# Performance work log

Measured on AMD Instinct MI355X. Metric: run time of the kernel, lower is better.

Reference implementation:

```python
import jax, jax.numpy as jnp
import numpy as np

B, NPG, H, HEADS, L, E, IN_DIM, FREQ = 4, 256, 128, 4, 6, 65536, 5, 256
N = B * NPG
C = H // HEADS  # per-head channels = 32


def _w(key, shape, fan_in):
    return jax.random.normal(key, shape, jnp.float32) * (fan_in ** -0.5)


def _ln(x):  # LayerNorm, elementwise_affine=False, eps=1e-5
    mu = jnp.mean(x, axis=-1, keepdims=True)
    var = jnp.mean((x - mu) ** 2, axis=-1, keepdims=True)
    return (x - mu) / jnp.sqrt(var + 1e-5)


def setup_inputs() -> dict:
    key = jax.random.key(0)
    ks = jax.random.split(key, 40)
    x = jax.random.normal(ks[0], (N, IN_DIM), jnp.float32)
    # edges constrained within each graph
    kg = jnp.repeat(jnp.arange(B), E // B)
    src = jax.random.randint(ks[1], (E,), 0, NPG) + kg * NPG
    dst = jax.random.randint(ks[2], (E,), 0, NPG) + kg * NPG
    edge_index = jnp.stack([src, dst]).astype(jnp.int32)
    batch = jnp.repeat(jnp.arange(B), NPG).astype(jnp.int32)
    time_matrix = jax.random.normal(ks[3], (N, N), jnp.float32)
    p = {}
    p['Wn'] = _w(ks[4], (IN_DIM, H), IN_DIM); p['bn'] = jnp.zeros((H,), jnp.float32)
    p['Wee'] = _w(ks[5], (1, 1), 1); p['bee'] = jnp.zeros((1,), jnp.float32)
    p['Wt1'] = _w(ks[6], (FREQ, H), FREQ); p['bt1'] = jnp.zeros((H,), jnp.float32)
    p['Wt2'] = _w(ks[7], (H, H), H); p['bt2'] = jnp.zeros((H,), jnp.float32)
    p['Wa'] = _w(ks[8], (L, H, 4 * H), H); p['ba'] = jnp.zeros((L, 4 * H), jnp.float32)
    p['Wq'] = _w(ks[9], (L, H, H), H); p['bq'] = jnp.zeros((L, H), jnp.float32)
    p['Wk'] = _w(ks[10], (L, H, H), H); p['bk'] = jnp.zeros((L, H), jnp.float32)
    p['Wv'] = _w(ks[11], (L, H, H), H); p['bv'] = jnp.zeros((L, H), jnp.float32)
    p['We'] = _w(ks[12], (L, 1, H), 1)  # lin_edge, bias=False in PyG
    p['Wskip'] = _w(ks[13], (L, H, H), H); p['bskip'] = jnp.zeros((L, H), jnp.float32)
    p['Wf1'] = _w(ks[14], (L, H, 2 * H), H); p['bf1'] = jnp.zeros((L, 2 * H), jnp.float32)
    p['Wf2'] = _w(ks[15], (L, 2 * H, H), 2 * H); p['bf2'] = jnp.zeros((L, H), jnp.float32)
    p['Wb'] = _w(ks[16], (H, H, H), H); p['bb'] = jnp.zeros((H,), jnp.float32)
    p['Wm1'] = _w(ks[17], (H, H), H); p['bm1'] = jnp.zeros((H,), jnp.float32)
    p['Wm2'] = _w(ks[18], (H, 4), H); p['bm2'] = jnp.zeros((4,), jnp.float32)
    return {'x': x, 'edge_index': edge_index, 'batch': batch, 't': 50,
            'time_matrix': time_matrix, **p}


def reference(x, edge_index, batch, t, time_matrix,
              Wn, bn, Wee, bee, Wt1, bt1, Wt2, bt2,
              Wa, ba, Wq, bq, Wk, bk, Wv, bv, We, Wskip, bskip,
              Wf1, bf1, Wf2, bf2, Wb, bb, Wm1, bm1, Wm2, bm2):
    h = x @ Wn + bn  # [N,H]
    # sinusoidal timestep embedding (dim=FREQ)
    half = FREQ // 2
    freqs = jnp.exp(-jnp.log(jnp.float32(10000.0)) * jnp.arange(half, dtype=jnp.float32) / half)
    targs = jnp.float32(t) * freqs
    emb = jnp.concatenate([jnp.cos(targs), jnp.sin(targs)])[None, :]  # [1,FREQ]
    t_emb = jax.nn.silu(emb @ Wt1 + bt1) @ Wt2 + bt2  # [1,H]
    t_mod = jax.nn.silu(t_emb)

    src, dst = edge_index[0], edge_index[1]
    edge_attr = time_matrix[src, dst][:, None] @ Wee + bee  # [E,1]

    inv_sqrt_c = jnp.float32(1.0 / np.sqrt(C))
    for l in range(L):
        ss = t_mod @ Wa[l] + ba[l]  # [1,4H]
        sh_msa, sc_msa, sh_mlp, sc_mlp = jnp.split(ss, 4, axis=1)
        hn = _ln(h) * (1 + sc_msa) + sh_msa
        # TransformerConv: gather per-edge Q/K/V, softmax over incoming edges of dst
        q = (hn @ Wq[l] + bq[l]).reshape(N, HEADS, C)
        k = (hn @ Wk[l] + bk[l]).reshape(N, HEADS, C)
        v = (hn @ Wv[l] + bv[l]).reshape(N, HEADS, C)
        e = (edge_attr @ We[l]).reshape(E, HEADS, C)
        kj = k[src] + e
        alpha = jnp.sum(q[dst] * kj, axis=-1) * inv_sqrt_c  # [E,HEADS]
        m = jax.ops.segment_max(alpha, dst, num_segments=N)
        a = jnp.exp(alpha - m[dst])
        s = jax.ops.segment_sum(a, dst, num_segments=N)
        a = a / (s[dst] + 1e-16)
        msg = (v[src] + e) * a[..., None]  # [E,HEADS,C]
        attn_out = jax.ops.segment_sum(msg, dst, num_segments=N).reshape(N, H)
        attn_out = attn_out + hn @ Wskip[l] + bskip[l]  # root/skip connection
        h = h + attn_out
        hn = _ln(h) * (1 + sc_mlp) + sh_mlp
        h = h + (jax.nn.gelu(hn @ Wf1[l] + bf1[l], approximate=False) @ Wf2[l] + bf2[l])

    # to_dense_batch: all graphs have NPG nodes -> reshape, full mask
    hd = h.reshape(B, NPG, H)
    # nn.Bilinear: pair[b,i,j,o] = h[b,i] @ Wb[o] @ h[b,j] + bb[o]
    tmp = jnp.einsum('bik,okl->biol', hd, Wb)  # [B,n,H,H]
    pair = jnp.einsum('biol,bjl->bijo', tmp, hd) + bb  # [B,n,n,H]
    logits = jax.nn.silu(pair @ Wm1 + bm1) @ Wm2 + bm2  # [B,n,n,4]
    return logits
```

## Files before the change

kernel.cpp:

```cpp
#include <hip/hip_runtime.h>
#include <math.h>

#define N_NODES 1024
#define HDIM 128
#define EDGES 65536
#define LAYERS 6

typedef __attribute__((ext_vector_type(8))) short bf16x8;
typedef __attribute__((ext_vector_type(4))) float f32x4;

#define OFF_H     0
#define OFF_Q     131072
#define OFF_K     262144
#define OFF_V     393216
#define OFF_SKP   524288
#define OFF_G     655360
#define OFF_SS    917504
#define OFF_EA    920576
#define OFF_CVEC  986112
#define OFF_INT   986240
#define OFF_M     1054912
#define OFF_U     3152064
#define OFF_MT    11540672
#define OFF_HB    12589248
#define OFF_WB    12654912

#define WM1T_OFF  786432

__device__ __forceinline__ float silu_f(float x) { return x / (1.f + expf(-x)); }
__device__ __forceinline__ float frcp(float x) { return __builtin_amdgcn_rcpf(x); }

__device__ __forceinline__ unsigned short f2bf(float f) {
    unsigned int u = __float_as_uint(f);
    u += 0x7FFFu + ((u >> 16) & 1u);
    return (unsigned short)(u >> 16);
}
__device__ __forceinline__ float bf2f(unsigned short s) {
    return __uint_as_float(((unsigned int)s) << 16);
}

__global__ __launch_bounds__(256) void k_ssf(const void* tptr,
    const float* __restrict__ Wt1, const float* __restrict__ bt1,
    const float* __restrict__ Wt2, const float* __restrict__ bt2,
    const float* __restrict__ bb, const float* __restrict__ Wm1, const float* __restrict__ bm1,
    const float* __restrict__ Wa, const float* __restrict__ ba,
    float* __restrict__ ss_all, float* __restrict__ cvec)
{
    __shared__ float emb_s[256];
    __shared__ float part[2][128];
    __shared__ float tmp1_s[128];
    __shared__ float tmod_s[128];
    int tid = threadIdx.x;
    int iv = *(const int*)tptr;
    float fv = __int_as_float(iv);
    float tval = (iv > -1000000 && iv < 1000000) ? (float)iv : fv;
    {
        int fi = tid & 127;
        float fr = expf(-logf(10000.f) * (float)fi / 128.f);
        float ta = tval * fr;
        emb_s[tid] = (tid < 128) ? cosf(ta) : sinf(ta);
    }
    __syncthreads();
    {
        int col = tid & 127, sl = tid >> 7;
        float p = 0.f;
#pragma unroll 8
        for (int i = sl * 128; i < sl * 128 + 128; i++) p += emb_s[i] * Wt1[i * 128 + col];
        part[sl][col] = p;
    }
    __syncthreads();
    if (tid < 128) tmp1_s[tid] = silu_f(bt1[tid] + part[0][tid] + part[1][tid]);
    __syncthreads();
    {
        int col = tid & 127, sl = tid >> 7;
        float p = 0.f;
#pragma unroll 8
        for (int i = sl * 64; i < sl * 64 + 64; i++) p += tmp1_s[i] * Wt2[i * 128 + col];
        part[sl][col] = p;
    }
    __syncthreads();
    if (tid < 128) tmod_s[tid] = silu_f(bt2[tid] + part[0][tid] + part[1][tid]);
    __syncthreads();
    {
        int idx = blockIdx.x * 256 + tid;
        int l = idx >> 9, j = idx & 511;
        float a = ba[l * 512 + j];
        const float* w = Wa + l * 65536 + j;
#pragma unroll 4
        for (int k = 0; k < 128; k++) a += tmod_s[k] * w[k * 512];
        ss_all[idx] = a;
    }
    if (blockIdx.x == 0) {
        {
            int col = tid & 127, sl = tid >> 7;
            float p = 0.f;
#pragma unroll 8
            for (int i = sl * 64; i < sl * 64 + 64; i++) p += bb[i] * Wm1[i * 128 + col];
            part[sl][col] = p;
        }
        __syncthreads();
        if (tid < 128) cvec[tid] = bm1[tid] + part[0][tid] + part[1][tid];
    }
}

__global__ __launch_bounds__(256) void k_wtrans(
    const float* __restrict__ Wq, const float* __restrict__ Wk,
    const float* __restrict__ Wv, const float* __restrict__ Wsk,
    const float* __restrict__ Wf1, const float* __restrict__ Wf2,
    const float* __restrict__ Wm1, short* __restrict__ WT)
{
    __shared__ __align__(16) short T[64][80];
    int t = blockIdx.x;
    int tid = threadIdx.x;
    const float* src; short* dst; int K, N, kt, nt;
    if (t < 96) {
        int mat = t >> 2, sub = t & 3;
        int l = mat >> 2, m = mat & 3;
        src = (m == 0 ? Wq : m == 1 ? Wk : m == 2 ? Wv : Wsk) + l * 16384;
        dst = WT + (size_t)mat * 16384;
        K = 128; N = 128; kt = sub >> 1; nt = sub & 1;
    } else if (t < 144) {
        int i = t - 96; int l = i >> 3, sub = i & 7;
        src = Wf1 + l * 32768;
        dst = WT + 24 * 16384 + (size_t)l * 32768;
        K = 128; N = 256; kt = sub & 1; nt = sub >> 1;
    } else if (t < 192) {
        int i = t - 144; int l = i >> 3, sub = i & 7;
        src = Wf2 + l * 32768;
        dst = WT + 24 * 16384 + 6 * 32768 + (size_t)l * 32768;
        K = 256; N = 128; kt = sub >> 1; nt = sub & 1;
    } else {
        int sub = t - 192;
        src = Wm1;
        dst = WT + WM1T_OFF;
        K = 128; N = 128; kt = sub >> 1; nt = sub & 1;
    }
    int k0 = kt * 64, n0 = nt * 64;
    for (int p = 0; p < 16; p++) {
        int idx = p * 256 + tid;
        int kk = idx >> 6, nn = idx & 63;
        T[nn][kk] = (short)f2bf(src[(k0 + kk) * N + n0 + nn]);
    }
    __syncthreads();
    for (int p = 0; p < 2; p++) {
        int idx = p * 256 + tid;
        int nn = idx >> 3, sq = idx & 7;
        *(int4*)&dst[(size_t)(n0 + nn) * K + k0 + sq * 8] = *(const int4*)&T[nn][sq * 8];
    }
}

__global__ __launch_bounds__(256) void k_inpedge(const float* __restrict__ x,
    const float* __restrict__ Wn, const float* __restrict__ bn, float* __restrict__ h,
    const int* __restrict__ ei, const float* __restrict__ tm,
    const float* __restrict__ Wee, const float* __restrict__ bee,
    float* __restrict__ ea, int* __restrict__ deg)
{
    int bid = blockIdx.x;
    int tid = threadIdx.x;
    if (bid < 512) {
        int idx = bid * 256 + tid;
        int i = idx >> 7, j = idx & 127;
        float acc = bn[j];
#pragma unroll
        for (int kk = 0; kk < 5; kk++) acc += x[i * 5 + kk] * Wn[kk * 128 + j];
        h[idx] = acc;
    } else {
        int e = (bid - 512) * 256 + tid;
        int s = ei[e], d = ei[EDGES + e];
        ea[e] = tm[s * N_NODES + d] * Wee[0] + bee[0];
        atomicAdd(&deg[d], 1);
    }
}

__global__ __launch_bounds__(1024) void k_scan(const int* __restrict__ deg, int* __restrict__ rowptr)
{
    __shared__ int tmp[1024];
    int tid = threadIdx.x;
    tmp[tid] = deg[tid];
    __syncthreads();
    for (int off = 1; off < 1024; off <<= 1) {
        int vv = (tid >= off) ? tmp[tid - off] : 0;
        __syncthreads();
        tmp[tid] += vv;
        __syncthreads();
    }
    rowptr[tid + 1] = tmp[tid];
    if (tid == 0) rowptr[0] = 0;
}

__global__ __launch_bounds__(256) void k_scatter(const int* __restrict__ ei,
    const int* __restrict__ rowptr, int* __restrict__ cursor, int* __restrict__ eorder)
{
    int e = blockIdx.x * 256 + threadIdx.x;
    int d = ei[EDGES + e];
    int pos = atomicAdd(&cursor[d], 1);
    eorder[rowptr[d] + pos] = e;
}

__global__ __launch_bounds__(128) void k_sort2(const int* __restrict__ rowptr,
    int* __restrict__ eorder, const int* __restrict__ ei, const float* __restrict__ ea,
    int* __restrict__ src_csr, float* __restrict__ ea_csr)
{
    __shared__ int key[256];
    int node = blockIdx.x;
    int tid = threadIdx.x;
    int beg = rowptr[node], end = rowptr[node + 1];
    int n = end - beg;
    if (n <= 256) {
        for (int i = tid; i < 256; i += 128) key[i] = (i < n) ? eorder[beg + i] : 0x7FFFFFFF;
        __syncthreads();
        for (int k = 2; k <= 256; k <<= 1) {
            for (int j = k >> 1; j > 0; j >>= 1) {
                int i = ((tid / j) * 2 * j) + (tid % j);
                int l = i + j;
                bool up = ((i & k) == 0);
                int a = key[i], b = key[l];
                if ((a > b) == up) { key[i] = b; key[l] = a; }
                __syncthreads();
            }
        }
        for (int i = tid; i < n; i += 128) {
            int e = key[i];
            src_csr[beg + i] = ei[e];
            ea_csr[beg + i] = ea[e];
        }
    } else {
        if (tid == 0) {
            for (int i = beg + 1; i < end; ++i) {
                int kk = eorder[i];
                int j = i - 1;
                while (j >= beg && eorder[j] > kk) { eorder[j + 1] = eorder[j]; --j; }
                eorder[j + 1] = kk;
            }
        }
        __syncthreads();
        for (int i = tid; i < n; i += 128) {
            int e = eorder[beg + i];
            src_csr[beg + i] = ei[e];
            ea_csr[beg + i] = ea[e];
        }
    }
}

__global__ __launch_bounds__(256) void k_qkvs(const float* __restrict__ h,
    const float* __restrict__ ss, const short* __restrict__ WT, int layer,
    const float* __restrict__ bq, const float* __restrict__ bk,
    const float* __restrict__ bv, const float* __restrict__ bsk,
    float* __restrict__ q, short* __restrict__ kb16, short* __restrict__ vb16,
    float* __restrict__ skp)
{
    __shared__ __align__(16) short As[16][136];
    __shared__ float shs[128], scs[128];
    int tid = threadIdx.x;
    int r0 = blockIdx.x * 16;
    if (tid < 128) { shs[tid] = ss[tid]; scs[tid] = ss[128 + tid]; }
    __syncthreads();
    {
        int row = tid >> 4, o = tid & 15;
        const float* hr = h + (size_t)(r0 + row) * 128 + o * 8;
        float s = 0.f, s2 = 0.f;
#pragma unroll
        for (int j = 0; j < 2; j++) {
            float4 vv = *(const float4*)&hr[j * 4];
            s += vv.x + vv.y + vv.z + vv.w;
            s2 += vv.x * vv.x + vv.y * vv.y + vv.z * vv.z + vv.w * vv.w;
        }
        s += __shfl_xor(s, 1, 64); s2 += __shfl_xor(s2, 1, 64);
        s += __shfl_xor(s, 2, 64); s2 += __shfl_xor(s2, 2, 64);
        s += __shfl_xor(s, 4, 64); s2 += __shfl_xor(s2, 4, 64);
        s += __shfl_xor(s, 8, 64); s2 += __shfl_xor(s2, 8, 64);
        float mu = s * (1.f / 128.f);
        float var = s2 * (1.f / 128.f) - mu * mu;
        float rs = rsqrtf(var + 1e-5f);
#pragma unroll
        for (int j = 0; j < 2; j++) {
            float4 vv = *(const float4*)&hr[j * 4];
            int cb = o * 8 + j * 4;
            short4 o4;
            o4.x = (short)f2bf((vv.x - mu) * rs * (1.f + scs[cb])     + shs[cb]);
            o4.y = (short)f2bf((vv.y - mu) * rs * (1.f + scs[cb + 1]) + shs[cb + 1]);
            o4.z = (short)f2bf((vv.z - mu) * rs * (1.f + scs[cb + 2]) + shs[cb + 2]);
            o4.w = (short)f2bf((vv.w - mu) * rs * (1.f + scs[cb + 3]) + shs[cb + 3]);
            *(short4*)&As[row][cb] = o4;
        }
    }
    __syncthreads();
    int w = tid >> 6, lane = tid & 63, c = lane & 15, g = lane >> 4;
    const short* Wm = WT + (size_t)(layer * 4 + w) * 16384;
    f32x4 acc[8] = {};
#pragma unroll
    for (int kq = 0; kq < 4; kq++) {
        int ko = kq * 32 + g * 8;
        bf16x8 a0 = *(const bf16x8*)&As[c][ko];
#pragma unroll
        for (int nt = 0; nt < 8; nt++) {
            bf16x8 bfr = *(const bf16x8*)&Wm[(size_t)(nt * 16 + c) * 128 + ko];
            acc[nt] = __builtin_amdgcn_mfma_f32_16x16x32_bf16(a0, bfr, acc[nt], 0, 0, 0);
        }
    }
    if (w == 0) {
#pragma unroll
        for (int nt = 0; nt < 8; nt++) {
            int n = nt * 16 + c;
            float bv2 = bq[n];
#pragma unroll
            for (int r = 0; r < 4; r++)
                q[(size_t)(r0 + g * 4 + r) * 128 + n] = acc[nt][r] + bv2;
        }
    } else if (w == 1) {
#pragma unroll
        for (int nt = 0; nt < 8; nt++) {
            int n = nt * 16 + c;
            float bv2 = bk[n];
#pragma unroll
            for (int r = 0; r < 4; r++)
                kb16[(size_t)(r0 + g * 4 + r) * 128 + n] = (short)f2bf(acc[nt][r] + bv2);
        }
    } else if (w == 2) {
#pragma unroll
        for (int nt = 0; nt < 8; nt++) {
            int n = nt * 16 + c;
            float bv2 = bv[n];
#pragma unroll
            for (int r = 0; r < 4; r++)
                vb16[(size_t)(r0 + g * 4 + r) * 128 + n] = (short)f2bf(acc[nt][r] + bv2);
        }
    } else {
#pragma unroll
        for (int nt = 0; nt < 8; nt++) {
            int n = nt * 16 + c;
            float bv2 = bsk[n];
#pragma unroll
            for (int r = 0; r < 4; r++)
                skp[(size_t)(r0 + g * 4 + r) * 128 + n] = acc[nt][r] + bv2;
        }
    }
}

__global__ __launch_bounds__(256) void k_ffn(float* __restrict__ h,
    const short* __restrict__ WT, int layer,
    const float* __restrict__ bf1, const float* __restrict__ bf2,
    const float* __restrict__ ss2, short* __restrict__ hb, int last)
{
    __shared__ __align__(16) short As[16][136];
    __shared__ __align__(16) short Gs[16][264];
    __shared__ float shs[128], scs[128];
    int tid = threadIdx.x;
    int r0 = blockIdx.x * 16;
    if (tid < 128) { shs[tid] = ss2[tid]; scs[tid] = ss2[128 + tid]; }
    __syncthreads();
    {
        int row = tid >> 4, o = tid & 15;
        const float* hr = h + (size_t)(r0 + row) * 128 + o * 8;
        float s = 0.f, s2 = 0.f;
#pragma unroll
        for (int j = 0; j < 2; j++) {
            float4 vv = *(const float4*)&hr[j * 4];
            s += vv.x + vv.y + vv.z + vv.w;
            s2 += vv.x * vv.x + vv.y * vv.y + vv.z * vv.z + vv.w * vv.w;
        }
        s += __shfl_xor(s, 1, 64); s2 += __shfl_xor(s2, 1, 64);
        s += __shfl_xor(s, 2, 64); s2 += __shfl_xor(s2, 2, 64);
        s += __shfl_xor(s, 4, 64); s2 += __shfl_xor(s2, 4, 64);
        s += __shfl_xor(s, 8, 64); s2 += __shfl_xor(s2, 8, 64);
        float mu = s * (1.f / 128.f);
        float var = s2 * (1.f / 128.f) - mu * mu;
        float rs = rsqrtf(var + 1e-5f);
#pragma unroll
        for (int j = 0; j < 2; j++) {
            float4 vv = *(const float4*)&hr[j * 4];
            int cb = o * 8 + j * 4;
            short4 o4;
            o4.x = (short)f2bf((vv.x - mu) * rs * (1.f + scs[cb])     + shs[cb]);
            o4.y = (short)f2bf((vv.y - mu) * rs * (1.f + scs[cb + 1]) + shs[cb + 1]);
            o4.z = (short)f2bf((vv.z - mu) * rs * (1.f + scs[cb + 2]) + shs[cb + 2]);
            o4.w = (short)f2bf((vv.w - mu) * rs * (1.f + scs[cb + 3]) + shs[cb + 3]);
            *(short4*)&As[row][cb] = o4;
        }
    }
    __syncthreads();
    int w = tid >> 6, lane = tid & 63, c = lane & 15, g = lane >> 4;
    const short* W1 = WT + 24 * 16384 + (size_t)layer * 32768;
    const short* W2 = WT + 24 * 16384 + 6 * 32768 + (size_t)layer * 32768;
    {
        f32x4 acc[4] = {};
#pragma unroll
        for (int kq = 0; kq < 4; kq++) {
            int ko = kq * 32 + g * 8;
            bf16x8 a0 = *(const bf16x8*)&As[c][ko];
#pragma unroll
            for (int nt = 0; nt < 4; nt++) {
                bf16x8 bfr = *(const bf16x8*)&W1[(size_t)(w * 64 + nt * 16 + c) * 128 + ko];
                acc[nt] = __builtin_amdgcn_mfma_f32_16x16x32_bf16(a0, bfr, acc[nt], 0, 0, 0);
            }
        }
#pragma unroll
        for (int nt = 0; nt < 4; nt++) {
            int n = w * 64 + nt * 16 + c;
            float bv = bf1[n];
#pragma unroll
            for (int r = 0; r < 4; r++) {
                float y = acc[nt][r] + bv;
                float gl = 0.5f * y * (1.f + erff(y * 0.70710678118654752f));
                Gs[g * 4 + r][n] = (short)f2bf(gl);
            }
        }
    }
    __syncthreads();
    {
        f32x4 acc2[2] = {};
#pragma unroll
        for (int kq = 0; kq < 8; kq++) {
            int ko = kq * 32 + g * 8;
            bf16x8 a0 = *(const bf16x8*)&Gs[c][ko];
#pragma unroll
            for (int nt2 = 0; nt2 < 2; nt2++) {
                bf16x8 bfr = *(const bf16x8*)&W2[(size_t)(w * 32 + nt2 * 16 + c) * 256 + ko];
                acc2[nt2] = __builtin_amdgcn_mfma_f32_16x16x32_bf16(a0, bfr, acc2[nt2], 0, 0, 0);
            }
        }
#pragma unroll
        for (int nt2 = 0; nt2 < 2; nt2++) {
            int n = w * 32 + nt2 * 16 + c;
            float bv = bf2[n];
#pragma unroll
            for (int r = 0; r < 4; r++) {
                int i = r0 + g * 4 + r;
                float nv = h[(size_t)i * 128 + n] + acc2[nt2][r] + bv;
                h[(size_t)i * 128 + n] = nv;
                if (last) hb[(size_t)i * 128 + n] = (short)f2bf(nv);
            }
        }
    }
}

__global__ __launch_bounds__(256) void k_attn(const float* __restrict__ q,
    const short* __restrict__ kb16, const short* __restrict__ vb16,
    const float* __restrict__ skp, float* __restrict__ h,
    const int* __restrict__ src_csr, const float* __restrict__ ea_csr,
    const float* __restrict__ We_l, const int* __restrict__ rowptr)
{
    __shared__ float ms[3][64], ssb[3][64], a0s[3][64], a1s[3][64];
    int tid = threadIdx.x;
    int wid = tid >> 6;
    int lane = tid & 63;
    int node = blockIdx.x;
    int c0 = lane * 2;
    float2 q2 = *(const float2*)&q[node * 128 + c0];
    float we0 = We_l[c0], we1 = We_l[c0 + 1];
    int beg = rowptr[node], end = rowptr[node + 1];
    int n = end - beg;
    int tb = beg + (n * wid) / 4;
    int te = beg + (n * (wid + 1)) / 4;
    float m = -INFINITY, s = 0.f, a0 = 0.f, a1 = 0.f;
    const float isc = 0.17677669529663687f;

    int t = tb;
    for (; t + 3 < te; t += 4) {
        int sn0 = src_csr[t],     sn1 = src_csr[t + 1];
        int sn2 = src_csr[t + 2], sn3 = src_csr[t + 3];
        float e0 = ea_csr[t],     e1 = ea_csr[t + 1];
        float e2 = ea_csr[t + 2], e3 = ea_csr[t + 3];
        ushort2 ku0 = *(const ushort2*)&kb16[sn0 * 128 + c0];
        ushort2 ku1 = *(const ushort2*)&kb16[sn1 * 128 + c0];
        ushort2 ku2 = *(const ushort2*)&kb16[sn2 * 128 + c0];
        ushort2 ku3 = *(const ushort2*)&kb16[sn3 * 128 + c0];
        ushort2 vu0 = *(const ushort2*)&vb16[sn0 * 128 + c0];
        ushort2 vu1 = *(const ushort2*)&vb16[sn1 * 128 + c0];
        ushort2 vu2 = *(const ushort2*)&vb16[sn2 * 128 + c0];
        ushort2 vu3 = *(const ushort2*)&vb16[sn3 * 128 + c0];
        float p0 = q2.x * (bf2f(ku0.x) + e0 * we0) + q2.y * (bf2f(ku0.y) + e0 * we1);
        float p1 = q2.x * (bf2f(ku1.x) + e1 * we0) + q2.y * (bf2f(ku1.y) + e1 * we1);
        float p2 = q2.x * (bf2f(ku2.x) + e2 * we0) + q2.y * (bf2f(ku2.y) + e2 * we1);
        float p3 = q2.x * (bf2f(ku3.x) + e3 * we0) + q2.y * (bf2f(ku3.y) + e3 * we1);
        p0 += __shfl_xor(p0, 1, 16); p1 += __shfl_xor(p1, 1, 16);
        p2 += __shfl_xor(p2, 1, 16); p3 += __shfl_xor(p3, 1, 16);
        p0 += __shfl_xor(p0, 2, 16); p1 += __shfl_xor(p1, 2, 16);
        p2 += __shfl_xor(p2, 2, 16); p3 += __shfl_xor(p3, 2, 16);
        p0 += __shfl_xor(p0, 4, 16); p1 += __shfl_xor(p1, 4, 16);
        p2 += __shfl_xor(p2, 4, 16); p3 += __shfl_xor(p3, 4, 16);
        p0 += __shfl_xor(p0, 8, 16); p1 += __shfl_xor(p1, 8, 16);
        p2 += __shfl_xor(p2, 8, 16); p3 += __shfl_xor(p3, 8, 16);
        {
            float al = p0 * isc;
            float mn = fmaxf(m, al);
            float scale = __expf(m - mn), wq = __expf(al - mn);
            s = s * scale + wq;
            a0 = a0 * scale + wq * (bf2f(vu0.x) + e0 * we0);
            a1 = a1 * scale + wq * (bf2f(vu0.y) + e0 * we1);
            m = mn;
        }
        {
            float al = p1 * isc;
            float mn = fmaxf(m, al);
            float scale = __expf(m - mn), wq = __expf(al - mn);
            s = s * scale + wq;
            a0 = a0 * scale + wq * (bf2f(vu1.x) + e1 * we0);
            a1 = a1 * scale + wq * (bf2f(vu1.y) + e1 * we1);
            m = mn;
        }
        {
            float al = p2 * isc;
            float mn = fmaxf(m, al);
            float scale = __expf(m - mn), wq = __expf(al - mn);
            s = s * scale + wq;
            a0 = a0 * scale + wq * (bf2f(vu2.x) + e2 * we0);
            a1 = a1 * scale + wq * (bf2f(vu2.y) + e2 * we1);
            m = mn;
        }
        {
            float al = p3 * isc;
            float mn = fmaxf(m, al);
            float scale = __expf(m - mn), wq = __expf(al - mn);
            s = s * scale + wq;
            a0 = a0 * scale + wq * (bf2f(vu3.x) + e3 * we0);
            a1 = a1 * scale + wq * (bf2f(vu3.y) + e3 * we1);
            m = mn;
        }
    }
    for (; t < te; ++t) {
        int sn = src_csr[t];
        float eav = ea_csr[t];
        ushort2 ku = *(const ushort2*)&kb16[sn * 128 + c0];
        ushort2 vu = *(const ushort2*)&vb16[sn * 128 + c0];
        float part = q2.x * (bf2f(ku.x) + eav * we0) + q2.y * (bf2f(ku.y) + eav * we1);
        part += __shfl_xor(part, 1, 16);
        part += __shfl_xor(part, 2, 16);
        part += __shfl_xor(part, 4, 16);
        part += __shfl_xor(part, 8, 16);
        float alpha = part * isc;
        float mn = fmaxf(m, alpha);
        float scale = __expf(m - mn), wq = __expf(alpha - mn);
        s = s * scale + wq;
        a0 = a0 * scale + wq * (bf2f(vu.x) + eav * we0);
        a1 = a1 * scale + wq * (bf2f(vu.y) + eav * we1);
        m = mn;
    }
    if (wid > 0) {
        ms[wid - 1][lane] = m; ssb[wid - 1][lane] = s;
        a0s[wid - 1][lane] = a0; a1s[wid - 1][lane] = a1;
    }
    __syncthreads();
    if (wid == 0) {
#pragma unroll
        for (int p = 0; p < 3; p++) {
            float mB = ms[p][lane], sB = ssb[p][lane];
            float b0 = a0s[p][lane], b1 = a1s[p][lane];
            float mm = fmaxf(m, mB);
            float eA = (m  > -1e30f) ? __expf(m  - mm) : 0.f;
            float eB = (mB > -1e30f) ? __expf(mB - mm) : 0.f;
            s = s * eA + sB * eB;
            a0 = a0 * eA + b0 * eB;
            a1 = a1 * eA + b1 * eB;
            m = mm;
        }
        float inv = (s > 0.f) ? 1.f / (s + 1e-16f) : 0.f;
        int o = node * 128 + c0;
        h[o]     += skp[o]     + a0 * inv;
        h[o + 1] += skp[o + 1] + a1 * inv;
    }
}

__global__ __launch_bounds__(256) void k_mprep(const float* __restrict__ Wb,
    const short* __restrict__ WT, float* __restrict__ M)
{
    __shared__ __align__(16) short Bls[128][136];
    int tid = threadIdx.x;
    int k = blockIdx.x;
    const short* Wm1T = WT + WM1T_OFF;
    {
        int lq = (tid & 31) * 4;
        int ob = tid >> 5;
        for (int it = 0; it < 16; it++) {
            int o = it * 8 + ob;
            float4 vv = *(const float4*)&Wb[(size_t)o * 16384 + k * 128 + lq];
            Bls[lq][o]     = (short)f2bf(vv.x);
            Bls[lq + 1][o] = (short)f2bf(vv.y);
            Bls[lq + 2][o] = (short)f2bf(vv.z);
            Bls[lq + 3][o] = (short)f2bf(vv.w);
        }
    }
    __syncthreads();
    int w = tid >> 6, lane = tid & 63, c = lane & 15, g = lane >> 4;
    f32x4 acc[2][8] = {};
#pragma unroll
    for (int kq = 0; kq < 4; kq++) {
        int ko = kq * 32 + g * 8;
        bf16x8 a0 = *(const bf16x8*)&Wm1T[(size_t)(w * 32 + c) * 128 + ko];
        bf16x8 a1 = *(const bf16x8*)&Wm1T[(size_t)(w * 32 + 16 + c) * 128 + ko];
#pragma unroll
        for (int nt = 0; nt < 8; nt++) {
            bf16x8 b = *(const bf16x8*)&Bls[nt * 16 + c][ko];
            acc[0][nt] = __builtin_amdgcn_mfma_f32_16x16x32_bf16(a0, b, acc[0][nt], 0, 0, 0);
            acc[1][nt] = __builtin_amdgcn_mfma_f32_16x16x32_bf16(a1, b, acc[1][nt], 0, 0, 0);
        }
    }
    float* Mk = M + (size_t)k * 16384;
#pragma unroll
    for (int it = 0; it < 2; it++)
#pragma unroll
        for (int nt = 0; nt < 8; nt++)
#pragma unroll
            for (int r = 0; r < 4; r++) {
                int m = w * 32 + it * 16 + g * 4 + r;
                int l = nt * 16 + c;
                Mk[m * 128 + l] = acc[it][nt][r];
            }
}

__global__ __launch_bounds__(256) void k_mtrans(const float* __restrict__ M,
                                                short* __restrict__ Mt)
{
    __shared__ __align__(16) short Ts[64][136];
    int tid = threadIdx.x;
    int n0 = blockIdx.x * 64;
    for (int p = 0; p < 32; p++) {
        int idx = p * 256 + tid;
        int k = idx >> 6, nn = idx & 63;
        Ts[nn][k] = (short)f2bf(M[(size_t)k * 16384 + n0 + nn]);
    }
    __syncthreads();
    for (int p = 0; p < 4; p++) {
        int idx = p * 256 + tid;
        int nn = idx >> 4, s = idx & 15;
        *(int4*)&Mt[(size_t)(n0 + nn) * 128 + s * 8] = *(const int4*)&Ts[nn][s * 8];
    }
}

__global__ __launch_bounds__(256) void k_p1(const short* __restrict__ hb,
    const short* __restrict__ Mt, short* __restrict__ U)
{
    __shared__ __align__(16) short As[128][72];
    __shared__ __align__(16) short Bs[128][72];
    int tid = threadIdx.x;
    int n0 = blockIdx.x * 128;
    int i0 = blockIdx.y * 128;
    int w = tid >> 6, lane = tid & 63, c = lane & 15, g = lane >> 4;
    f32x4 acc[2][8] = {};
    for (int kh = 0; kh < 2; kh++) {
        __syncthreads();
        for (int idx = tid; idx < 1024; idx += 256) {
            int r = idx >> 3, s = idx & 7;
            *(int4*)&As[r][s * 8] = *(const int4*)&hb[(i0 + r) * 128 + kh * 64 + s * 8];
            *(int4*)&Bs[r][s * 8] = *(const int4*)&Mt[(size_t)(n0 + r) * 128 + kh * 64 + s * 8];
        }
        __syncthreads();
#pragma unroll
        for (int kk = 0; kk < 2; kk++) {
            int ko = kk * 32 + g * 8;
            bf16x8 a0 = *(const bf16x8*)&As[w * 32 + c][ko];
            bf16x8 a1 = *(const bf16x8*)&As[w * 32 + 16 + c][ko];
#pragma unroll
            for (int nt = 0; nt < 8; nt++) {
                bf16x8 b = *(const bf16x8*)&Bs[nt * 16 + c][ko];
                acc[0][nt] = __builtin_amdgcn_mfma_f32_16x16x32_bf16(a0, b, acc[0][nt], 0, 0, 0);
                acc[1][nt] = __builtin_amdgcn_mfma_f32_16x16x32_bf16(a1, b, acc[1][nt], 0, 0, 0);
            }
        }
    }
#pragma unroll
    for (int it = 0; it < 2; it++)
#pragma unroll
        for (int nt = 0; nt < 8; nt++)
#pragma unroll
            for (int r = 0; r < 4; r++) {
                int i = i0 + w * 32 + it * 16 + g * 4 + r;
                int n = n0 + nt * 16 + c;
                U[(size_t)i * 16384 + n] = (short)f2bf(acc[it][nt][r]);
            }
}

__global__ __launch_bounds__(256) void k_p2(const short* __restrict__ hb,
    const short* __restrict__ U, const float* __restrict__ cvec,
    const float* __restrict__ Wm2, const float* __restrict__ bm2,
    float* __restrict__ out)
{
    __shared__ __align__(16) short Us[128][128];
    __shared__ float cvs[128];
    __shared__ float w2s[128][4];
    int tid = threadIdx.x;
    int i = blockIdx.x;
    int jb = blockIdx.y;
    int b = i >> 8;
    int w = tid >> 6, lane = tid & 63, c = lane & 15, g = lane >> 4;
    if (tid < 128) {
        cvs[tid] = cvec[tid];
        *(float4*)&w2s[tid][0] = *(const float4*)&Wm2[tid * 4];
    }
    bf16x8 hf[2][4];
    {
        const short* hrow = hb + (size_t)(b * 256 + jb * 128 + w * 32 + c) * 128;
#pragma unroll
        for (int jt = 0; jt < 2; jt++)
#pragma unroll
            for (int kq = 0; kq < 4; kq++)
                hf[jt][kq] = *(const bf16x8*)(hrow + jt * 16 * 128 + kq * 32 + g * 8);
    }
    for (int idx = tid; idx < 2048; idx += 256) {
        int r = idx >> 4, s = idx & 15;
        int col = (s * 8) ^ ((r & 7) << 3);
        *(int4*)&Us[r][col] = *(const int4*)&U[(size_t)i * 16384 + r * 128 + s * 8];
    }
    __syncthreads();
    f32x4 acc[2][8] = {};
#pragma unroll
    for (int kq = 0; kq < 4; kq++) {
        int ko = kq * 32 + g * 8;
#pragma unroll
        for (int mt = 0; mt < 8; mt++) {
            int row = mt * 16 + c;
            int col = ko ^ ((row & 7) << 3);
            bf16x8 uv = *(const bf16x8*)&Us[row][col];
            acc[0][mt] = __builtin_amdgcn_mfma_f32_16x16x32_bf16(uv, hf[0][kq], acc[0][mt], 0, 0, 0);
            acc[1][mt] = __builtin_amdgcn_mfma_f32_16x16x32_bf16(uv, hf[1][kq], acc[1][mt], 0, 0, 0);
        }
    }
    float4 bmv = *(const float4*)&bm2[0];
#pragma unroll
    for (int jt = 0; jt < 2; jt++) {
        float p0 = 0.f, p1 = 0.f, p2 = 0.f, p3 = 0.f;
#pragma unroll
        for (int mt = 0; mt < 8; mt++) {
#pragma unroll
            for (int r = 0; r < 4; r++) {
                int m = mt * 16 + g * 4 + r;
                float y = acc[jt][mt][r] + cvs[m];
                float sv = y * frcp(1.f + __expf(-y));
                p0 += sv * w2s[m][0]; p1 += sv * w2s[m][1];
                p2 += sv * w2s[m][2]; p3 += sv * w2s[m][3];
            }
        }
        p0 += __shfl_xor(p0, 16, 64); p1 += __shfl_xor(p1, 16, 64);
        p2 += __shfl_xor(p2, 16, 64); p3 += __shfl_xor(p3, 16, 64);
        p0 += __shfl_xor(p0, 32, 64); p1 += __shfl_xor(p1, 32, 64);
        p2 += __shfl_xor(p2, 32, 64); p3 += __shfl_xor(p3, 32, 64);
        if (g == 0) {
            int j = jb * 128 + w * 32 + jt * 16 + c;
            float4 o4 = { p0 + bmv.x, p1 + bmv.y, p2 + bmv.z, p3 + bmv.w };
            *(float4*)&out[((size_t)i * 256 + j) * 4] = o4;
        }
    }
}

extern "C" void kernel_launch(void* const* d_in, const int* in_sizes, int n_in,
                              void* d_out, int out_size, void* d_ws, size_t ws_size,
                              hipStream_t stream)
{
    const float* x   = (const float*)d_in[0];
    const int*   ei  = (const int*)d_in[1];
    const void*  tptr= d_in[3];
    const float* tm  = (const float*)d_in[4];
    const float* Wn  = (const float*)d_in[5];
    const float* bn  = (const float*)d_in[6];
    const float* Wee = (const float*)d_in[7];
    const float* bee = (const float*)d_in[8];
    const float* Wt1 = (const float*)d_in[9];
    const float* bt1 = (const float*)d_in[10];
    const float* Wt2 = (const float*)d_in[11];
    const float* bt2 = (const float*)d_in[12];
    const float* Wa  = (const float*)d_in[13];
    const float* ba  = (const float*)d_in[14];
    const float* Wq  = (const float*)d_in[15];
    const float* bq  = (const float*)d_in[16];
    const float* Wk  = (const float*)d_in[17];
    const float* bk  = (const float*)d_in[18];
    const float* Wv  = (const float*)d_in[19];
    const float* bv  = (const float*)d_in[20];
    const float* We  = (const float*)d_in[21];
    const float* Wsk = (const float*)d_in[22];
    const float* bsk = (const float*)d_in[23];
    const float* Wf1 = (const float*)d_in[24];
    const float* bf1 = (const float*)d_in[25];
    const float* Wf2 = (const float*)d_in[26];
    const float* bf2 = (const float*)d_in[27];
    const float* Wb  = (const float*)d_in[28];
    const float* bb  = (const float*)d_in[29];
    const float* Wm1 = (const float*)d_in[30];
    const float* bm1 = (const float*)d_in[31];
    const float* Wm2 = (const float*)d_in[32];
    const float* bm2 = (const float*)d_in[33];
    float* out = (float*)d_out;
    float* ws = (float*)d_ws;

    float* h    = ws + OFF_H;
    float* qb   = ws + OFF_Q;
    short* kb16 = (short*)(ws + OFF_K);
    short* vb16 = (short*)(ws + OFF_V);
    float* skp  = ws + OFF_SKP;
    float* ss   = ws + OFF_SS;
    float* ea   = ws + OFF_EA;
    float* cvec = ws + OFF_CVEC;
    int* iws    = (int*)(ws + OFF_INT);
    int* deg    = iws;
    int* cursor = iws + 1024;
    int* rowptr = iws + 2048;
    int* eorder = iws + 3073;
    int* src_csr   = (int*)(ws + OFF_G);
    float* ea_csr  = ws + OFF_G + 65536;
    float* Mst  = ws + OFF_M;
    short* Ub   = (short*)(ws + OFF_U);
    short* Mtb  = (short*)(ws + OFF_MT);
    short* hbb  = (short*)(ws + OFF_HB);
    short* WT   = (short*)(ws + OFF_WB);

    hipMemsetAsync(deg, 0, 2048 * sizeof(int), stream);
    k_ssf<<<12, 256, 0, stream>>>(tptr, Wt1, bt1, Wt2, bt2, bb, Wm1, bm1, Wa, ba, ss, cvec);
    k_wtrans<<<196, 256, 0, stream>>>(Wq, Wk, Wv, Wsk, Wf1, Wf2, Wm1, WT);
    k_inpedge<<<768, 256, 0, stream>>>(x, Wn, bn, h, ei, tm, Wee, bee, ea, deg);
    k_scan<<<1, 1024, 0, stream>>>(deg, rowptr);
    k_scatter<<<256, 256, 0, stream>>>(ei, rowptr, cursor, eorder);
    k_sort2<<<1024, 128, 0, stream>>>(rowptr, eorder, ei, ea, src_csr, ea_csr);

    for (int l = 0; l < LAYERS; l++) {
        const float* ssl = ss + l * 512;
        k_qkvs<<<64, 256, 0, stream>>>(h, ssl, WT, l,
            bq + l * 128, bk + l * 128, bv + l * 128, bsk + l * 128,
            qb, kb16, vb16, skp);
        k_attn<<<1024, 256, 0, stream>>>(qb, kb16, vb16, skp, h, src_csr, ea_csr,
                                         We + l * 128, rowptr);
        k_ffn<<<64, 256, 0, stream>>>(h, WT, l, bf1 + l * 256, bf2 + l * 128,
                                      ssl + 256, hbb, l == LAYERS - 1);
    }

    k_mprep<<<128, 256, 0, stream>>>(Wb, WT, Mst);
    k_mtrans<<<256, 256, 0, stream>>>(Mst, Mtb);
    k_p1<<<dim3(128, 8), 256, 0, stream>>>(hbb, Mtb, Ub);
    k_p2<<<dim3(1024, 2), 256, 0, stream>>>(hbb, Ub, cvec, Wm2, bm2, out);
}
```

Measured before the change: 276.3 us.

## Merge setup kernels and weight-product prep into one launch, swap grid axes

Folds the time-embedding/scale-shift kernel, the weight transpose kernel, the input/edge kernel, and the bilinear M-prep kernel into one multi-role kernel. Block index selects the role. The M-prep branch now builds its own transposed bf16 Wm1 tile in shared memory instead of reading the transposed weights, which removes its dependency on the transpose blocks. Grid axes of the two pair kernels are swapped so that consecutive blocks walk the inner dimension. This saves three launches, but the fused kernel reserves ~68KB of shared memory for every block, which can lower occupancy for the lightweight elementwise blocks.

```diff
diff --git a/kernel.cpp b/kernel.cpp
--- a/kernel.cpp
+++ b/kernel.cpp
@@ -39,136 +39,184 @@
     return __uint_as_float(((unsigned int)s) << 16);
 }
 
-__global__ __launch_bounds__(256) void k_ssf(const void* tptr,
+__global__ __launch_bounds__(256) void k_setup_all(const void* tptr,
     const float* __restrict__ Wt1, const float* __restrict__ bt1,
     const float* __restrict__ Wt2, const float* __restrict__ bt2,
     const float* __restrict__ bb, const float* __restrict__ Wm1, const float* __restrict__ bm1,
     const float* __restrict__ Wa, const float* __restrict__ ba,
-    float* __restrict__ ss_all, float* __restrict__ cvec)
-{
-    __shared__ float emb_s[256];
-    __shared__ float part[2][128];
-    __shared__ float tmp1_s[128];
-    __shared__ float tmod_s[128];
+    float* __restrict__ ss_all, float* __restrict__ cvec,
+    const float* __restrict__ Wq, const float* __restrict__ Wk,
+    const float* __restrict__ Wv, const float* __restrict__ Wsk,
+    const float* __restrict__ Wf1, const float* __restrict__ Wf2,
+    short* __restrict__ WT,
+    const float* __restrict__ x, const float* __restrict__ Wn, const float* __restrict__ bn,
+    float* __restrict__ h, const int* __restrict__ ei, const float* __restrict__ tm,
+    const float* __restrict__ Wee, const float* __restrict__ bee,
+    float* __restrict__ ea, int* __restrict__ deg,
+    const float* __restrict__ Wb, float* __restrict__ M)
+{
+    __shared__ __align__(16) char smem[69632];
+    int bid = blockIdx.x;
     int tid = threadIdx.x;
-    int iv = *(const int*)tptr;
-    float fv = __int_as_float(iv);
-    float tval = (iv > -1000000 && iv < 1000000) ? (float)iv : fv;
-    {
-        int fi = tid & 127;
-        float fr = expf(-logf(10000.f) * (float)fi / 128.f);
-        float ta = tval * fr;
-        emb_s[tid] = (tid < 128) ? cosf(ta) : sinf(ta);
-    }
-    __syncthreads();
-    {
-        int col = tid & 127, sl = tid >> 7;
-        float p = 0.f;
-#pragma unroll 8
-        for (int i = sl * 128; i < sl * 128 + 128; i++) p += emb_s[i] * Wt1[i * 128 + col];
-        part[sl][col] = p;
-    }
-    __syncthreads();
-    if (tid < 128) tmp1_s[tid] = silu_f(bt1[tid] + part[0][tid] + part[1][tid]);
-    __syncthreads();
-    {
-        int col = tid & 127, sl = tid >> 7;
-        float p = 0.f;
-#pragma unroll 8
-        for (int i = sl * 64; i < sl * 64 + 64; i++) p += tmp1_s[i] * Wt2[i * 128 + col];
-        part[sl][col] = p;
-    }
-    __syncthreads();
-    if (tid < 128) tmod_s[tid] = silu_f(bt2[tid] + part[0][tid] + part[1][tid]);
-    __syncthreads();
-    {
-        int idx = blockIdx.x * 256 + tid;
-        int l = idx >> 9, j = idx & 511;
-        float a = ba[l * 512 + j];
-        const float* w = Wa + l * 65536 + j;
-#pragma unroll 4
-        for (int k = 0; k < 128; k++) a += tmod_s[k] * w[k * 512];
-        ss_all[idx] = a;
-    }
-    if (blockIdx.x == 0) {
+
+    if (bid < 12) {
+        float* emb_s  = (float*)smem;
+        float* part   = emb_s + 256;
+        float* tmp1_s = part + 256;
+        float* tmod_s = tmp1_s + 128;
+        int iv = *(const int*)tptr;
+        float fv = __int_as_float(iv);
+        float tval = (iv > -1000000 && iv < 1000000) ? (float)iv : fv;
+        {
+            int fi = tid & 127;
+            float fr = expf(-logf(10000.f) * (float)fi / 128.f);
+            float ta = tval * fr;
+            emb_s[tid] = (tid < 128) ? cosf(ta) : sinf(ta);
+        }
+        __syncthreads();
         {
             int col = tid & 127, sl = tid >> 7;
             float p = 0.f;
 #pragma unroll 8
-            for (int i = sl * 64; i < sl * 64 + 64; i++) p += bb[i] * Wm1[i * 128 + col];
-            part[sl][col] = p;
-        }
-        __syncthreads();
-        if (tid < 128) cvec[tid] = bm1[tid] + part[0][tid] + part[1][tid];
-    }
-}
-
-__global__ __launch_bounds__(256) void k_wtrans(
-    const float* __restrict__ Wq, const float* __restrict__ Wk,
-    const float* __restrict__ Wv, const float* __restrict__ Wsk,
-    const float* __restrict__ Wf1, const float* __restrict__ Wf2,
-    const float* __restrict__ Wm1, short* __restrict__ WT)
-{
-    __shared__ __align__(16) short T[64][80];
-    int t = blockIdx.x;
-    int tid = threadIdx.x;
-    const float* src; short* dst; int K, N, kt, nt;
-    if (t < 96) {
-        int mat = t >> 2, sub = t & 3;
-        int l = mat >> 2, m = mat & 3;
-        src = (m == 0 ? Wq : m == 1 ? Wk : m == 2 ? Wv : Wsk) + l * 16384;
-        dst = WT + (size_t)mat * 16384;
-        K = 128; N = 128; kt = sub >> 1; nt = sub & 1;
-    } else if (t < 144) {
-        int i = t - 96; int l = i >> 3, sub = i & 7;
-        src = Wf1 + l * 32768;
-        dst = WT + 24 * 16384 + (size_t)l * 32768;
-        K = 128; N = 256; kt = sub & 1; nt = sub >> 1;
-    } else if (t < 192) {
-        int i = t - 144; int l = i >> 3, sub = i & 7;
-        src = Wf2 + l * 32768;
-        dst = WT + 24 * 16384 + 6 * 32768 + (size_t)l * 32768;
-        K = 256; N = 128; kt = sub >> 1; nt = sub & 1;
+            for (int i = sl * 128; i < sl * 128 + 128; i++) p += emb_s[i] * Wt1[i * 128 + col];
+            part[sl * 128 + col] = p;
+        }
+        __syncthreads();
+        if (tid < 128) tmp1_s[tid] = silu_f(bt1[tid] + part[tid] + part[128 + tid]);
+        __syncthreads();
+        {
+            int col = tid & 127, sl = tid >> 7;
+            float p = 0.f;
+#pragma unroll 8
+            for (int i = sl * 64; i < sl * 64 + 64; i++) p += tmp1_s[i] * Wt2[i * 128 + col];
+            part[sl * 128 + col] = p;
+        }
+        __syncthreads();
+        if (tid < 128) tmod_s[tid] = silu_f(bt2[tid] + part[tid] + part[128 + tid]);
+        __syncthreads();
+        {
+            int idx = bid * 256 + tid;
+            int l = idx >> 9, j = idx & 511;
+            float a = ba[l * 512 + j];
+            const float* w = Wa + l * 65536 + j;
+#pragma unroll 4
+            for (int k = 0; k < 128; k++) a += tmod_s[k] * w[k * 512];
+            ss_all[idx] = a;
+        }
+        if (bid == 0) {
+            {
+                int col = tid & 127, sl = tid >> 7;
+                float p = 0.f;
+#pragma unroll 8
+                for (int i = sl * 64; i < sl * 64 + 64; i++) p += bb[i] * Wm1[i * 128 + col];
+                part[sl * 128 + col] = p;
+            }
+            __syncthreads();
+            if (tid < 128) cvec[tid] = bm1[tid] + part[tid] + part[128 + tid];
+        }
+    } else if (bid < 208) {
+        short (*T)[80] = (short(*)[80])smem;
+        int t = bid - 12;
+        const float* src; short* dst; int K, N, kt, nt;
+        if (t < 96) {
+            int mat = t >> 2, sub = t & 3;
+            int l = mat >> 2, m = mat & 3;
+            src = (m == 0 ? Wq : m == 1 ? Wk : m == 2 ? Wv : Wsk) + l * 16384;
+            dst = WT + (size_t)mat * 16384;
+            K = 128; N = 128; kt = sub >> 1; nt = sub & 1;
+        } else if (t < 144) {
+            int i = t - 96; int l = i >> 3, sub = i & 7;
+            src = Wf1 + l * 32768;
+            dst = WT + 24 * 16384 + (size_t)l * 32768;
+            K = 128; N = 256; kt = sub & 1; nt = sub >> 1;
+        } else if (t < 192) {
+            int i = t - 144; int l = i >> 3, sub = i & 7;
+            src = Wf2 + l * 32768;
+            dst = WT + 24 * 16384 + 6 * 32768 + (size_t)l * 32768;
+            K = 256; N = 128; kt = sub >> 1; nt = sub & 1;
+        } else {
+            int sub = t - 192;
+            src = Wm1;
+            dst = WT + WM1T_OFF;
+            K = 128; N = 128; kt = sub >> 1; nt = sub & 1;
+        }
+        int k0 = kt * 64, n0 = nt * 64;
+        for (int p = 0; p < 16; p++) {
+            int idx = p * 256 + tid;
+            int kk = idx >> 6, nn = idx & 63;
+            T[nn][kk] = (short)f2bf(src[(k0 + kk) * N + n0 + nn]);
+        }
+        __syncthreads();
+        for (int p = 0; p < 2; p++) {
+            int idx = p * 256 + tid;
+            int nn = idx >> 3, sq = idx & 7;
+            *(int4*)&dst[(size_t)(n0 + nn) * K + k0 + sq * 8] = *(const int4*)&T[nn][sq * 8];
+        }
+    } else if (bid < 976) {
+        int b2 = bid - 208;
+        if (b2 < 512) {
+            int idx = b2 * 256 + tid;
+            int i = idx >> 7, j = idx & 127;
+            float acc = bn[j];
+#pragma unroll
+            for (int kk = 0; kk < 5; kk++) acc += x[i * 5 + kk] * Wn[kk * 128 + j];
+            h[idx] = acc;
+        } else {
+            int e = (b2 - 512) * 256 + tid;
+            int s = ei[e], d = ei[EDGES + e];
+            ea[e] = tm[s * N_NODES + d] * Wee[0] + bee[0];
+            atomicAdd(&deg[d], 1);
+        }
     } else {
-        int sub = t - 192;
-        src = Wm1;
-        dst = WT + WM1T_OFF;
-        K = 128; N = 128; kt = sub >> 1; nt = sub & 1;
-    }
-    int k0 = kt * 64, n0 = nt * 64;
-    for (int p = 0; p < 16; p++) {
-        int idx = p * 256 + tid;
-        int kk = idx >> 6, nn = idx & 63;
-        T[nn][kk] = (short)f2bf(src[(k0 + kk) * N + n0 + nn]);
-    }
-    __syncthreads();
-    for (int p = 0; p < 2; p++) {
-        int idx = p * 256 + tid;
-        int nn = idx >> 3, sq = idx & 7;
-        *(int4*)&dst[(size_t)(n0 + nn) * K + k0 + sq * 8] = *(const int4*)&T[nn][sq * 8];
-    }
-}
-
-__global__ __launch_bounds__(256) void k_inpedge(const float* __restrict__ x,
-    const float* __restrict__ Wn, const float* __restrict__ bn, float* __restrict__ h,
-    const int* __restrict__ ei, const float* __restrict__ tm,
-    const float* __restrict__ Wee, const float* __restrict__ bee,
-    float* __restrict__ ea, int* __restrict__ deg)
-{
-    int bid = blockIdx.x;
-    int tid = threadIdx.x;
-    if (bid < 512) {
-        int idx = bid * 256 + tid;
-        int i = idx >> 7, j = idx & 127;
-        float acc = bn[j];
-#pragma unroll
-        for (int kk = 0; kk < 5; kk++) acc += x[i * 5 + kk] * Wn[kk * 128 + j];
-        h[idx] = acc;
-    } else {
-        int e = (bid - 512) * 256 + tid;
-        int s = ei[e], d = ei[EDGES + e];
-        ea[e] = tm[s * N_NODES + d] * Wee[0] + bee[0];
-        atomicAdd(&deg[d], 1);
+        short (*Bls)[136]   = (short(*)[136])smem;
+        short (*Wm1Tl)[136] = (short(*)[136])(smem + 34816);
+        int k = bid - 976;
+        {
+            int lq = (tid & 31) * 4;
+            int ob = tid >> 5;
+            for (int it = 0; it < 16; it++) {
+                int o = it * 8 + ob;
+                float4 vv = *(const float4*)&Wb[(size_t)o * 16384 + k * 128 + lq];
+                Bls[lq][o]     = (short)f2bf(vv.x);
+                Bls[lq + 1][o] = (short)f2bf(vv.y);
+                Bls[lq + 2][o] = (short)f2bf(vv.z);
+                Bls[lq + 3][o] = (short)f2bf(vv.w);
+            }
+        }
+        {
+            int m = tid & 127;
+            int oh = tid >> 7;
+            for (int it = 0; it < 64; it++) {
+                int o = it * 2 + oh;
+                Wm1Tl[m][o] = (short)f2bf(Wm1[o * 128 + m]);
+            }
+        }
+        __syncthreads();
+        int w = tid >> 6, lane = tid & 63, c = lane & 15, g = lane >> 4;
+        f32x4 acc[2][8] = {};
+#pragma unroll
+        for (int kq = 0; kq < 4; kq++) {
+            int ko = kq * 32 + g * 8;
+            bf16x8 a0 = *(const bf16x8*)&Wm1Tl[w * 32 + c][ko];
+            bf16x8 a1 = *(const bf16x8*)&Wm1Tl[w * 32 + 16 + c][ko];
+#pragma unroll
+            for (int nt = 0; nt < 8; nt++) {
+                bf16x8 b = *(const bf16x8*)&Bls[nt * 16 + c][ko];
+                acc[0][nt] = __builtin_amdgcn_mfma_f32_16x16x32_bf16(a0, b, acc[0][nt], 0, 0, 0);
+                acc[1][nt] = __builtin_amdgcn_mfma_f32_16x16x32_bf16(a1, b, acc[1][nt], 0, 0, 0);
+            }
+        }
+        float* Mk = M + (size_t)k * 16384;
+#pragma unroll
+        for (int it = 0; it < 2; it++)
+#pragma unroll
+            for (int nt = 0; nt < 8; nt++)
+#pragma unroll
+                for (int r = 0; r < 4; r++) {
+                    int m = w * 32 + it * 16 + g * 4 + r;
+                    int l = nt * 16 + c;
+                    Mk[m * 128 + l] = acc[it][nt][r];
+                }
     }
 }
 
@@ -561,53 +609,6 @@
     }
 }
 
-__global__ __launch_bounds__(256) void k_mprep(const float* __restrict__ Wb,
-    const short* __restrict__ WT, float* __restrict__ M)
-{
-    __shared__ __align__(16) short Bls[128][136];
-    int tid = threadIdx.x;
-    int k = blockIdx.x;
-    const short* Wm1T = WT + WM1T_OFF;
-    {
-        int lq = (tid & 31) * 4;
-        int ob = tid >> 5;
-        for (int it = 0; it < 16; it++) {
-            int o = it * 8 + ob;
-            float4 vv = *(const float4*)&Wb[(size_t)o * 16384 + k * 128 + lq];
-            Bls[lq][o]     = (short)f2bf(vv.x);
-            Bls[lq + 1][o] = (short)f2bf(vv.y);
-            Bls[lq + 2][o] = (short)f2bf(vv.z);
-            Bls[lq + 3][o] = (short)f2bf(vv.w);
-        }
-    }
-    __syncthreads();
-    int w = tid >> 6, lane = tid & 63, c = lane & 15, g = lane >> 4;
-    f32x4 acc[2][8] = {};
-#pragma unroll
-    for (int kq = 0; kq < 4; kq++) {
-        int ko = kq * 32 + g * 8;
-        bf16x8 a0 = *(const bf16x8*)&Wm1T[(size_t)(w * 32 + c) * 128 + ko];
-        bf16x8 a1 = *(const bf16x8*)&Wm1T[(size_t)(w * 32 + 16 + c) * 128 + ko];
-#pragma unroll
-        for (int nt = 0; nt < 8; nt++) {
-            bf16x8 b = *(const bf16x8*)&Bls[nt * 16 + c][ko];
-            acc[0][nt] = __builtin_amdgcn_mfma_f32_16x16x32_bf16(a0, b, acc[0][nt], 0, 0, 0);
-            acc[1][nt] = __builtin_amdgcn_mfma_f32_16x16x32_bf16(a1, b, acc[1][nt], 0, 0, 0);
-        }
-    }
-    float* Mk = M + (size_t)k * 16384;
-#pragma unroll
-    for (int it = 0; it < 2; it++)
-#pragma unroll
-        for (int nt = 0; nt < 8; nt++)
-#pragma unroll
-            for (int r = 0; r < 4; r++) {
-                int m = w * 32 + it * 16 + g * 4 + r;
-                int l = nt * 16 + c;
-                Mk[m * 128 + l] = acc[it][nt][r];
-            }
-}
-
 __global__ __launch_bounds__(256) void k_mtrans(const float* __restrict__ M,
                                                 short* __restrict__ Mt)
 {
@@ -633,8 +634,8 @@
     __shared__ __align__(16) short As[128][72];
     __shared__ __align__(16) short Bs[128][72];
     int tid = threadIdx.x;
-    int n0 = blockIdx.x * 128;
-    int i0 = blockIdx.y * 128;
+    int i0 = blockIdx.x * 128;
+    int n0 = blockIdx.y * 128;
     int w = tid >> 6, lane = tid & 63, c = lane & 15, g = lane >> 4;
     f32x4 acc[2][8] = {};
     for (int kh = 0; kh < 2; kh++) {
@@ -679,8 +680,8 @@
     __shared__ float cvs[128];
     __shared__ float w2s[128][4];
     int tid = threadIdx.x;
-    int i = blockIdx.x;
-    int jb = blockIdx.y;
+    int jb = blockIdx.x;
+    int i = blockIdx.y;
     int b = i >> 8;
     int w = tid >> 6, lane = tid & 63, c = lane & 15, g = lane >> 4;
     if (tid < 128) {
@@ -804,9 +805,9 @@
     short* WT   = (short*)(ws + OFF_WB);
 
     hipMemsetAsync(deg, 0, 2048 * sizeof(int), stream);
-    k_ssf<<<12, 256, 0, stream>>>(tptr, Wt1, bt1, Wt2, bt2, bb, Wm1, bm1, Wa, ba, ss, cvec);
-    k_wtrans<<<196, 256, 0, stream>>>(Wq, Wk, Wv, Wsk, Wf1, Wf2, Wm1, WT);
-    k_inpedge<<<768, 256, 0, stream>>>(x, Wn, bn, h, ei, tm, Wee, bee, ea, deg);
+    k_setup_all<<<1104, 256, 0, stream>>>(tptr, Wt1, bt1, Wt2, bt2, bb, Wm1, bm1, Wa, ba,
+                                          ss, cvec, Wq, Wk, Wv, Wsk, Wf1, Wf2, WT,
+                                          x, Wn, bn, h, ei, tm, Wee, bee, ea, deg, Wb, Mst);
     k_scan<<<1, 1024, 0, stream>>>(deg, rowptr);
     k_scatter<<<256, 256, 0, stream>>>(ei, rowptr, cursor, eorder);
     k_sort2<<<1024, 128, 0, stream>>>(rowptr, eorder, ei, ea, src_csr, ea_csr);
@@ -822,8 +823,7 @@
                                       ssl + 256, hbb, l == LAYERS - 1);
     }
 
-    k_mprep<<<128, 256, 0, stream>>>(Wb, WT, Mst);
     k_mtrans<<<256, 256, 0, stream>>>(Mst, Mtb);
-    k_p1<<<dim3(128, 8), 256, 0, stream>>>(hbb, Mtb, Ub);
-    k_p2<<<dim3(1024, 2), 256, 0, stream>>>(hbb, Ub, cvec, Wm2, bm2, out);
-}
+    k_p1<<<dim3(8, 128), 256, 0, stream>>>(hbb, Mtb, Ub);
+    k_p2<<<dim3(2, 1024), 256, 0, stream>>>(hbb, Ub, cvec, Wm2, bm2, out);
+}
```

New measurement: 261.3 us. 1.06x faster.
